# Kernel tuning notes

Hardware: AMD Instinct MI355X
Metric: run time of the kernel (lower is better)

The kernel has to match this reference:

```python
import jax, jax.numpy as jnp
import numpy as np

TEMPERATURE = 0.07  # init kwarg 'temperature'


def setup_inputs() -> dict:
    key = jax.random.key(0)
    k1, k2, k3 = jax.random.split(key, 3)
    N, E = 8192, 128
    return {
        "audio_embeds": jax.random.normal(k1, (N, E), dtype=jnp.float32),
        "text_embeds": jax.random.normal(k2, (N, E), dtype=jnp.float32),
        "fids": jax.random.randint(k3, (N,), 0, 4096),
    }


def reference(audio_embeds, text_embeds, fids):
    # Per-sample loop in the original is equivalent to a full NxN score matrix
    # with a symmetric fid-equality mask (diagonal always kept):
    #   row i valid set  = {j : fid[j] != fid[i]} U {i}
    # L_it(i) = CE over S[i, valid] with target i  (A_i vs sampled texts)
    # L_ai(i) = CE over S[valid, i] with target i  (sampled audios vs T_i)
    S = jnp.matmul(audio_embeds, text_embeds.T) / TEMPERATURE  # [N, N], S[j, i] = <A_j, T_i>/t
    N = S.shape[0]
    mask = (fids[:, None] != fids[None, :]) | jnp.eye(N, dtype=bool)  # symmetric
    neg = jnp.finfo(S.dtype).min
    Sm = jnp.where(mask, S, neg)
    diag = jnp.diagonal(S)
    L_it = jax.nn.logsumexp(Sm, axis=1) - diag  # row-wise CE at diagonal target
    L_ai = jax.nn.logsumexp(Sm, axis=0) - diag  # column-wise CE at diagonal target
    return jnp.mean(L_ai + L_it)
```

## Files before the change

kernel.cpp:

```cpp
#include <hip/hip_runtime.h>
#include <hip/hip_bf16.h>
#include <math.h>

#define NN 8192
#define EE 128

static constexpr float INV_T = 1.0f / 0.07f;
static constexpr float LOG2E = 1.4426950408889634f;
static constexpr float LN2   = 0.6931471805599453f;
static constexpr float SENT  = -3.0e38f;

typedef __attribute__((ext_vector_type(8))) short fragAB;
typedef __attribute__((ext_vector_type(4))) float f32x4;
typedef const __attribute__((address_space(1))) void gvoid;
typedef __attribute__((address_space(3))) void lvoid;

__device__ inline float fexp2(float x) { float r; asm("v_exp_f32 %0, %1" : "=v"(r) : "v"(x)); return r; }
__device__ inline float flog2(float x) { float r; asm("v_log_f32 %0, %1" : "=v"(r) : "v"(x)); return r; }

template<int CTRL>
__device__ inline float dpp_f(float x) {
  return __builtin_bit_cast(float,
      __builtin_amdgcn_update_dpp(0, __builtin_bit_cast(int, x), CTRL, 0xf, 0xf, true));
}
__device__ inline float red16_max(float x) {
  x = fmaxf(x, dpp_f<0xB1>(x));
  x = fmaxf(x, dpp_f<0x4E>(x));
  x = fmaxf(x, dpp_f<0x141>(x));
  x = fmaxf(x, dpp_f<0x140>(x));
  return x;
}
__device__ inline float red16_add(float x) {
  x += dpp_f<0xB1>(x); x += dpp_f<0x4E>(x); x += dpp_f<0x141>(x); x += dpp_f<0x140>(x);
  return x;
}

__device__ inline ushort f32_to_bf16_bits(float x) {
  union { float f; unsigned u; } c; c.f = x;
  unsigned u = c.u;
  u += 0x7fffu + ((u >> 16) & 1u);
  return (ushort)(u >> 16);
}

__global__ void lsl_cvt_kernel(const float* __restrict__ A, const float* __restrict__ T,
                               ushort* __restrict__ Ab, ushort* __restrict__ Tb,
                               float* __restrict__ diag) {
  const int t = blockIdx.x * 256 + threadIdx.x;
  const int i = t * 4;
  float4 a = *reinterpret_cast<const float4*>(A + i);
  float4 tt = *reinterpret_cast<const float4*>(T + i);
  ushort4 oa, ot;
  const float SC = INV_T * LOG2E;
  oa.x = f32_to_bf16_bits(a.x * SC); oa.y = f32_to_bf16_bits(a.y * SC);
  oa.z = f32_to_bf16_bits(a.z * SC); oa.w = f32_to_bf16_bits(a.w * SC);
  ot.x = f32_to_bf16_bits(tt.x); ot.y = f32_to_bf16_bits(tt.y);
  ot.z = f32_to_bf16_bits(tt.z); ot.w = f32_to_bf16_bits(tt.w);
  *reinterpret_cast<ushort4*>(Ab + i) = oa;
  *reinterpret_cast<ushort4*>(Tb + i) = ot;

  float pd = a.x * tt.x + a.y * tt.y + a.z * tt.z + a.w * tt.w;
  pd += __shfl_xor(pd, 1); pd += __shfl_xor(pd, 2); pd += __shfl_xor(pd, 4);
  pd += __shfl_xor(pd, 8); pd += __shfl_xor(pd, 16);
  if ((threadIdx.x & 31) == 0) diag[i >> 7] = pd * (INV_T * LOG2E);
}

#define MMAC(av, bv)                                                              \
  _Pragma("unroll") for (int fm = 0; fm < 4; ++fm)                                \
    _Pragma("unroll") for (int fn = 0; fn < 4; ++fn)                              \
      acc[fm][fn] = __builtin_amdgcn_mfma_f32_16x16x32_bf16(av[fm], bv[fn], acc[fm][fn], 0, 0, 0);

__global__ __launch_bounds__(256) void
lsl_tile_kernel(const ushort* __restrict__ Ab, const ushort* __restrict__ Tb,
                const int* __restrict__ fids,
                float2* __restrict__ rowp, float2* __restrict__ colp) {
  __shared__ ushort As[128 * 128];
  __shared__ ushort Bs[128 * 128];

  const int bid = blockIdx.x;
  const int swz = (bid & 7) * 512 + (bid >> 3);
  const int tm = swz >> 6, tn = swz & 63;
  const int tid = threadIdx.x;
  const int lane = tid & 63;
  const int wid  = tid >> 6;
  const int wm = wid >> 1, wn = wid & 1;
  const int rbase = tm * 128 + wm * 64;
  const int cbase = tn * 128 + wn * 64;
  const int lr = lane & 15, lg = lane >> 4;

  {
    const int trow = tid >> 4;
    const int scol = ((tid & 15) ^ trow) * 8;
    const ushort* gA = Ab + (size_t)(tm * 128 + trow) * EE + scol;
    const ushort* gB = Tb + (size_t)(tn * 128 + trow) * EE + scol;
#pragma unroll
    for (int i = 0; i < 8; ++i)
      __builtin_amdgcn_global_load_lds((gvoid*)(gA + (size_t)i * 16 * EE),
          (lvoid*)((char*)As + i * 4096 + wid * 1024), 16, 0, 0);
#pragma unroll
    for (int i = 0; i < 8; ++i)
      __builtin_amdgcn_global_load_lds((gvoid*)(gB + (size_t)i * 16 * EE),
          (lvoid*)((char*)Bs + i * 4096 + wid * 1024), 16, 0, 0);
  }
  __syncthreads();

  f32x4 acc[4][4] = {};
#pragma unroll
  for (int ks = 0; ks < 4; ++ks) {
    fragAB av[4], bv[4];
#pragma unroll
    for (int f = 0; f < 4; ++f) {
      av[f] = *reinterpret_cast<const fragAB*>(
          &As[(wm * 64 + f * 16 + lr) * 128 + (((ks * 4 + lg) ^ lr) * 8)]);
      bv[f] = *reinterpret_cast<const fragAB*>(
          &Bs[(wn * 64 + f * 16 + lr) * 128 + (((ks * 4 + lg) ^ lr) * 8)]);
    }
    MMAC(av, bv)
  }

  int fr[4][4], fc[4];
#pragma unroll
  for (int fm = 0; fm < 4; ++fm) {
    int4 v4 = *reinterpret_cast<const int4*>(fids + rbase + fm * 16 + lg * 4);
    fr[fm][0] = v4.x; fr[fm][1] = v4.y; fr[fm][2] = v4.z; fr[fm][3] = v4.w;
  }
#pragma unroll
  for (int fn = 0; fn < 4; ++fn) fc[fn] = fids[cbase + fn * 16 + lr];

  float e[4][4][4];
  const bool diagtile = (rbase == cbase);
#pragma unroll
  for (int fm = 0; fm < 4; ++fm)
#pragma unroll
    for (int fn = 0; fn < 4; ++fn)
#pragma unroll
      for (int r = 0; r < 4; ++r) {
        float v = acc[fm][fn][r];
        bool keep = (fr[fm][r] != fc[fn]) || (diagtile && fm == fn && lr == lg * 4 + r);
        e[fm][fn][r] = keep ? v : SENT;
      }

  float rm[4][4];
#pragma unroll
  for (int fm = 0; fm < 4; ++fm)
#pragma unroll
    for (int r = 0; r < 4; ++r)
      rm[fm][r] = fmaxf(fmaxf(e[fm][0][r], e[fm][1][r]),
                        fmaxf(e[fm][2][r], e[fm][3][r]));
#pragma unroll
  for (int fm = 0; fm < 4; ++fm)
#pragma unroll
    for (int r = 0; r < 4; ++r)
      rm[fm][r] = red16_max(rm[fm][r]);

  float rs[4][4];
#pragma unroll
  for (int fm = 0; fm < 4; ++fm)
#pragma unroll
    for (int r = 0; r < 4; ++r)
      rs[fm][r] = (fexp2(e[fm][0][r] - rm[fm][r]) + fexp2(e[fm][1][r] - rm[fm][r]))
                + (fexp2(e[fm][2][r] - rm[fm][r]) + fexp2(e[fm][3][r] - rm[fm][r]));
#pragma unroll
  for (int fm = 0; fm < 4; ++fm)
#pragma unroll
    for (int r = 0; r < 4; ++r)
      rs[fm][r] = red16_add(rs[fm][r]);

  const int rblk = tn * 2 + wn;
  if (lr == 0) {
#pragma unroll
    for (int fm = 0; fm < 4; ++fm)
#pragma unroll
      for (int r = 0; r < 4; ++r)
        rowp[(size_t)rblk * NN + (rbase + fm * 16 + lg * 4 + r)] = make_float2(rm[fm][r], rs[fm][r]);
  }

  float cm[4];
#pragma unroll
  for (int fn = 0; fn < 4; ++fn) {
    float m0 = fmaxf(fmaxf(e[0][fn][0], e[0][fn][1]), fmaxf(e[0][fn][2], e[0][fn][3]));
    float m1 = fmaxf(fmaxf(e[1][fn][0], e[1][fn][1]), fmaxf(e[1][fn][2], e[1][fn][3]));
    float m2 = fmaxf(fmaxf(e[2][fn][0], e[2][fn][1]), fmaxf(e[2][fn][2], e[2][fn][3]));
    float m3 = fmaxf(fmaxf(e[3][fn][0], e[3][fn][1]), fmaxf(e[3][fn][2], e[3][fn][3]));
    cm[fn] = fmaxf(fmaxf(m0, m1), fmaxf(m2, m3));
  }
  {
    float t0 = __shfl_xor(cm[0], 16), t1 = __shfl_xor(cm[1], 16),
          t2 = __shfl_xor(cm[2], 16), t3 = __shfl_xor(cm[3], 16);
    cm[0] = fmaxf(cm[0], t0); cm[1] = fmaxf(cm[1], t1);
    cm[2] = fmaxf(cm[2], t2); cm[3] = fmaxf(cm[3], t3);
    t0 = __shfl_xor(cm[0], 32); t1 = __shfl_xor(cm[1], 32);
    t2 = __shfl_xor(cm[2], 32); t3 = __shfl_xor(cm[3], 32);
    cm[0] = fmaxf(cm[0], t0); cm[1] = fmaxf(cm[1], t1);
    cm[2] = fmaxf(cm[2], t2); cm[3] = fmaxf(cm[3], t3);
  }
  float cs[4];
#pragma unroll
  for (int fn = 0; fn < 4; ++fn) {
    float s0 = (fexp2(e[0][fn][0] - cm[fn]) + fexp2(e[0][fn][1] - cm[fn]))
             + (fexp2(e[0][fn][2] - cm[fn]) + fexp2(e[0][fn][3] - cm[fn]));
    float s1 = (fexp2(e[1][fn][0] - cm[fn]) + fexp2(e[1][fn][1] - cm[fn]))
             + (fexp2(e[1][fn][2] - cm[fn]) + fexp2(e[1][fn][3] - cm[fn]));
    float s2 = (fexp2(e[2][fn][0] - cm[fn]) + fexp2(e[2][fn][1] - cm[fn]))
             + (fexp2(e[2][fn][2] - cm[fn]) + fexp2(e[2][fn][3] - cm[fn]));
    float s3 = (fexp2(e[3][fn][0] - cm[fn]) + fexp2(e[3][fn][1] - cm[fn]))
             + (fexp2(e[3][fn][2] - cm[fn]) + fexp2(e[3][fn][3] - cm[fn]));
    cs[fn] = (s0 + s1) + (s2 + s3);
  }
  {
    float t0 = __shfl_xor(cs[0], 16), t1 = __shfl_xor(cs[1], 16),
          t2 = __shfl_xor(cs[2], 16), t3 = __shfl_xor(cs[3], 16);
    cs[0] += t0; cs[1] += t1; cs[2] += t2; cs[3] += t3;
    t0 = __shfl_xor(cs[0], 32); t1 = __shfl_xor(cs[1], 32);
    t2 = __shfl_xor(cs[2], 32); t3 = __shfl_xor(cs[3], 32);
    cs[0] += t0; cs[1] += t1; cs[2] += t2; cs[3] += t3;
  }

  const int cblk = tm * 2 + wm;
  if (lg == 0) {
#pragma unroll
    for (int fn = 0; fn < 4; ++fn)
      colp[(size_t)cblk * NN + (cbase + fn * 16 + lr)] = make_float2(cm[fn], cs[fn]);
  }
}

__global__ __launch_bounds__(256) void
lsl_merge_kernel(const float2* __restrict__ rowp, const float2* __restrict__ colp,
                 const float* __restrict__ diag, float* __restrict__ bsum) {
  __shared__ float2 sl[128 * 33];
  __shared__ float2 red[32][8];
  const int tid = threadIdx.x;
  const int ibase = blockIdx.x * 32;
  const int s = tid & 31, p = tid >> 5;

  float lse0 = 0.f, lse1 = 0.f;
#pragma unroll
  for (int pass = 0; pass < 2; ++pass) {
    const float2* __restrict__ src = pass ? colp : rowp;
#pragma unroll
    for (int k = 0; k < 16; ++k) {
      int L = tid + k * 256;
      int b = L >> 5, di = L & 31;
      sl[b * 33 + di] = src[(size_t)b * NN + ibase + di];
    }
    __syncthreads();
    float m = SENT;
#pragma unroll
    for (int k = 0; k < 16; ++k) m = fmaxf(m, sl[(p * 16 + k) * 33 + s].x);
    float sum = 0.f;
#pragma unroll
    for (int k = 0; k < 16; ++k) {
      float2 v = sl[(p * 16 + k) * 33 + s];
      sum += v.y * fexp2(v.x - m);
    }
    red[s][p] = make_float2(m, sum);
    __syncthreads();
    if (p == 0) {
      float M = SENT;
#pragma unroll
      for (int k = 0; k < 8; ++k) M = fmaxf(M, red[s][k].x);
      float S = 0.f;
#pragma unroll
      for (int k = 0; k < 8; ++k) S += red[s][k].y * fexp2(red[s][k].x - M);
      if (pass == 0) lse0 = M + flog2(S); else lse1 = M + flog2(S);
    }
    __syncthreads();
  }

  if (tid < 32) {
    float loss = lse0 + lse1 - 2.f * diag[ibase + tid];
#pragma unroll
    for (int d = 1; d < 32; d <<= 1) loss += __shfl_xor(loss, d);
    if (tid == 0) bsum[blockIdx.x] = loss;
  }
}

__global__ __launch_bounds__(256) void
lsl_final_kernel(const float* __restrict__ bsum, float* __restrict__ out) {
  float v = bsum[threadIdx.x];
#pragma unroll
  for (int d = 1; d < 64; d <<= 1) v += __shfl_xor(v, d);
  __shared__ float l4[4];
  if ((threadIdx.x & 63) == 0) l4[threadIdx.x >> 6] = v;
  __syncthreads();
  if (threadIdx.x == 0) out[0] = (l4[0] + l4[1] + l4[2] + l4[3]) * (LN2 / (float)NN);
}

extern "C" void kernel_launch(void* const* d_in, const int* in_sizes, int n_in,
                              void* d_out, int out_size, void* d_ws, size_t ws_size,
                              hipStream_t stream) {
  const float* A = (const float*)d_in[0];
  const float* T = (const float*)d_in[1];
  const int* fids = (const int*)d_in[2];
  float* out = (float*)d_out;
  char* ws = (char*)d_ws;

  size_t off = 0;
  ushort* Ab  = (ushort*)(ws + off); off += (size_t)NN * EE * 2;
  ushort* Tb  = (ushort*)(ws + off); off += (size_t)NN * EE * 2;
  float* diag = (float*)(ws + off);  off += (size_t)NN * 4;
  float2* rowp = (float2*)(ws + off); off += (size_t)NN * 128 * 8;
  float2* colp = (float2*)(ws + off); off += (size_t)NN * 128 * 8;
  float* bsum = (float*)(ws + off);  off += 1024;

  hipLaunchKernelGGL(lsl_cvt_kernel, dim3(NN * EE / 4 / 256), dim3(256), 0, stream, A, T, Ab, Tb, diag);
  hipLaunchKernelGGL(lsl_tile_kernel, dim3(4096), dim3(256), 0, stream, Ab, Tb, fids, rowp, colp);
  hipLaunchKernelGGL(lsl_merge_kernel, dim3(NN / 32), dim3(256), 0, stream, rowp, colp, diag, bsum);
  hipLaunchKernelGGL(lsl_final_kernel, dim3(1), dim3(256), 0, stream, bsum, out);
}
```

Measured before the change: 62.36 us.

## Split 128x128 tile across 8 waves with LDS merge of column partials

Raises the tile kernel from 4 to 8 waves per block. Each wave now computes a 32x64 sub-tile instead of 64x64, which halves the accumulator and exp work per wave and the registers it needs. Column partial max/sum pairs from the two waves sharing a column block are combined through a small shared-memory buffer with an extra barrier, so the colp layout stays the same. The aim is more latency hiding and occupancy. The cost is more B-fragment LDS reads per output and an extra sync.

Result: slower. 63.65 us (+2.1%).

```diff
diff --git a/kernel.cpp b/kernel.cpp
--- a/kernel.cpp
+++ b/kernel.cpp
@@ -64,17 +64,13 @@
   if ((threadIdx.x & 31) == 0) diag[i >> 7] = pd * (INV_T * LOG2E);
 }
 
-#define MMAC(av, bv)                                                              \
-  _Pragma("unroll") for (int fm = 0; fm < 4; ++fm)                                \
-    _Pragma("unroll") for (int fn = 0; fn < 4; ++fn)                              \
-      acc[fm][fn] = __builtin_amdgcn_mfma_f32_16x16x32_bf16(av[fm], bv[fn], acc[fm][fn], 0, 0, 0);
-
-__global__ __launch_bounds__(256) void
+__global__ __launch_bounds__(512, 4) void
 lsl_tile_kernel(const ushort* __restrict__ Ab, const ushort* __restrict__ Tb,
                 const int* __restrict__ fids,
                 float2* __restrict__ rowp, float2* __restrict__ colp) {
   __shared__ ushort As[128 * 128];
   __shared__ ushort Bs[128 * 128];
+  __shared__ float2 cscr[4 * 64];
 
   const int bid = blockIdx.x;
   const int swz = (bid & 7) * 512 + (bid >> 3);
@@ -82,85 +78,92 @@
   const int tid = threadIdx.x;
   const int lane = tid & 63;
   const int wid  = tid >> 6;
-  const int wm = wid >> 1, wn = wid & 1;
-  const int rbase = tm * 128 + wm * 64;
+  const int wm = wid >> 1;
+  const int wn = wid & 1;
+  const int rbase = tm * 128 + wm * 32;
   const int cbase = tn * 128 + wn * 64;
   const int lr = lane & 15, lg = lane >> 4;
 
   {
     const int trow = tid >> 4;
-    const int scol = ((tid & 15) ^ trow) * 8;
+    const int scol = ((tid & 15) ^ (trow & 15)) * 8;
     const ushort* gA = Ab + (size_t)(tm * 128 + trow) * EE + scol;
     const ushort* gB = Tb + (size_t)(tn * 128 + trow) * EE + scol;
 #pragma unroll
-    for (int i = 0; i < 8; ++i)
-      __builtin_amdgcn_global_load_lds((gvoid*)(gA + (size_t)i * 16 * EE),
-          (lvoid*)((char*)As + i * 4096 + wid * 1024), 16, 0, 0);
-#pragma unroll
-    for (int i = 0; i < 8; ++i)
-      __builtin_amdgcn_global_load_lds((gvoid*)(gB + (size_t)i * 16 * EE),
-          (lvoid*)((char*)Bs + i * 4096 + wid * 1024), 16, 0, 0);
+    for (int i = 0; i < 4; ++i)
+      __builtin_amdgcn_global_load_lds((gvoid*)(gA + (size_t)i * 32 * EE),
+          (lvoid*)((char*)As + i * 8192 + wid * 1024), 16, 0, 0);
+#pragma unroll
+    for (int i = 0; i < 4; ++i)
+      __builtin_amdgcn_global_load_lds((gvoid*)(gB + (size_t)i * 32 * EE),
+          (lvoid*)((char*)Bs + i * 8192 + wid * 1024), 16, 0, 0);
   }
   __syncthreads();
 
-  f32x4 acc[4][4] = {};
+  f32x4 acc[2][4] = {};
 #pragma unroll
   for (int ks = 0; ks < 4; ++ks) {
-    fragAB av[4], bv[4];
-#pragma unroll
-    for (int f = 0; f < 4; ++f) {
+    fragAB av[2], bv[4];
+#pragma unroll
+    for (int f = 0; f < 2; ++f)
       av[f] = *reinterpret_cast<const fragAB*>(
-          &As[(wm * 64 + f * 16 + lr) * 128 + (((ks * 4 + lg) ^ lr) * 8)]);
+          &As[(wm * 32 + f * 16 + lr) * 128 + (((ks * 4 + lg) ^ lr) * 8)]);
+#pragma unroll
+    for (int f = 0; f < 4; ++f)
       bv[f] = *reinterpret_cast<const fragAB*>(
           &Bs[(wn * 64 + f * 16 + lr) * 128 + (((ks * 4 + lg) ^ lr) * 8)]);
-    }
-    MMAC(av, bv)
-  }
-
-  int fr[4][4], fc[4];
-#pragma unroll
-  for (int fm = 0; fm < 4; ++fm) {
+#pragma unroll
+    for (int fm = 0; fm < 2; ++fm)
+#pragma unroll
+      for (int fn = 0; fn < 4; ++fn)
+        acc[fm][fn] = __builtin_amdgcn_mfma_f32_16x16x32_bf16(av[fm], bv[fn], acc[fm][fn], 0, 0, 0);
+  }
+
+  int fr[2][4], fc[4];
+#pragma unroll
+  for (int fm = 0; fm < 2; ++fm) {
     int4 v4 = *reinterpret_cast<const int4*>(fids + rbase + fm * 16 + lg * 4);
     fr[fm][0] = v4.x; fr[fm][1] = v4.y; fr[fm][2] = v4.z; fr[fm][3] = v4.w;
   }
 #pragma unroll
   for (int fn = 0; fn < 4; ++fn) fc[fn] = fids[cbase + fn * 16 + lr];
 
-  float e[4][4][4];
-  const bool diagtile = (rbase == cbase);
-#pragma unroll
-  for (int fm = 0; fm < 4; ++fm)
+  float e[2][4][4];
+  const bool dt = (tm == tn) && ((wm >> 1) == wn);
+  const int dfb = (wm & 1) * 2;
+#pragma unroll
+  for (int fm = 0; fm < 2; ++fm)
 #pragma unroll
     for (int fn = 0; fn < 4; ++fn)
 #pragma unroll
       for (int r = 0; r < 4; ++r) {
         float v = acc[fm][fn][r];
-        bool keep = (fr[fm][r] != fc[fn]) || (diagtile && fm == fn && lr == lg * 4 + r);
+        bool keep = (fr[fm][r] != fc[fn]) || (dt && fn == dfb + fm && lr == lg * 4 + r);
         e[fm][fn][r] = keep ? v : SENT;
       }
 
-  float rm[4][4];
-#pragma unroll
-  for (int fm = 0; fm < 4; ++fm)
+  float rm[2][4];
+#pragma unroll
+  for (int fm = 0; fm < 2; ++fm)
 #pragma unroll
     for (int r = 0; r < 4; ++r)
       rm[fm][r] = fmaxf(fmaxf(e[fm][0][r], e[fm][1][r]),
                         fmaxf(e[fm][2][r], e[fm][3][r]));
 #pragma unroll
-  for (int fm = 0; fm < 4; ++fm)
+  for (int fm = 0; fm < 2; ++fm)
 #pragma unroll
     for (int r = 0; r < 4; ++r)
       rm[fm][r] = red16_max(rm[fm][r]);
 
-  float rs[4][4];
-#pragma unroll
-  for (int fm = 0; fm < 4; ++fm)
+  float rs[2][4];
+#pragma unroll
+  for (int fm = 0; fm < 2; ++fm)
 #pragma unroll
     for (int r = 0; r < 4; ++r)
       rs[fm][r] = (fexp2(e[fm][0][r] - rm[fm][r]) + fexp2(e[fm][1][r] - rm[fm][r]))
                 + (fexp2(e[fm][2][r] - rm[fm][r]) + fexp2(e[fm][3][r] - rm[fm][r]));
 #pragma unroll
-  for (int fm = 0; fm < 4; ++fm)
+  for (int fm = 0; fm < 2; ++fm)
 #pragma unroll
     for (int r = 0; r < 4; ++r)
       rs[fm][r] = red16_add(rs[fm][r]);
@@ -168,7 +171,7 @@
   const int rblk = tn * 2 + wn;
   if (lr == 0) {
 #pragma unroll
-    for (int fm = 0; fm < 4; ++fm)
+    for (int fm = 0; fm < 2; ++fm)
 #pragma unroll
       for (int r = 0; r < 4; ++r)
         rowp[(size_t)rblk * NN + (rbase + fm * 16 + lg * 4 + r)] = make_float2(rm[fm][r], rs[fm][r]);
@@ -179,9 +182,7 @@
   for (int fn = 0; fn < 4; ++fn) {
     float m0 = fmaxf(fmaxf(e[0][fn][0], e[0][fn][1]), fmaxf(e[0][fn][2], e[0][fn][3]));
     float m1 = fmaxf(fmaxf(e[1][fn][0], e[1][fn][1]), fmaxf(e[1][fn][2], e[1][fn][3]));
-    float m2 = fmaxf(fmaxf(e[2][fn][0], e[2][fn][1]), fmaxf(e[2][fn][2], e[2][fn][3]));
-    float m3 = fmaxf(fmaxf(e[3][fn][0], e[3][fn][1]), fmaxf(e[3][fn][2], e[3][fn][3]));
-    cm[fn] = fmaxf(fmaxf(m0, m1), fmaxf(m2, m3));
+    cm[fn] = fmaxf(m0, m1);
   }
   {
     float t0 = __shfl_xor(cm[0], 16), t1 = __shfl_xor(cm[1], 16),
@@ -200,11 +201,7 @@
              + (fexp2(e[0][fn][2] - cm[fn]) + fexp2(e[0][fn][3] - cm[fn]));
     float s1 = (fexp2(e[1][fn][0] - cm[fn]) + fexp2(e[1][fn][1] - cm[fn]))
              + (fexp2(e[1][fn][2] - cm[fn]) + fexp2(e[1][fn][3] - cm[fn]));
-    float s2 = (fexp2(e[2][fn][0] - cm[fn]) + fexp2(e[2][fn][1] - cm[fn]))
-             + (fexp2(e[2][fn][2] - cm[fn]) + fexp2(e[2][fn][3] - cm[fn]));
-    float s3 = (fexp2(e[3][fn][0] - cm[fn]) + fexp2(e[3][fn][1] - cm[fn]))
-             + (fexp2(e[3][fn][2] - cm[fn]) + fexp2(e[3][fn][3] - cm[fn]));
-    cs[fn] = (s0 + s1) + (s2 + s3);
+    cs[fn] = s0 + s1;
   }
   {
     float t0 = __shfl_xor(cs[0], 16), t1 = __shfl_xor(cs[1], 16),
@@ -215,11 +212,22 @@
     cs[0] += t0; cs[1] += t1; cs[2] += t2; cs[3] += t3;
   }
 
-  const int cblk = tm * 2 + wm;
-  if (lg == 0) {
+  const int pi = (wm >> 1) * 2 + wn;
+  if ((wm & 1) == 1 && lg == 0) {
 #pragma unroll
     for (int fn = 0; fn < 4; ++fn)
-      colp[(size_t)cblk * NN + (cbase + fn * 16 + lr)] = make_float2(cm[fn], cs[fn]);
+      cscr[pi * 64 + fn * 16 + lr] = make_float2(cm[fn], cs[fn]);
+  }
+  __syncthreads();
+  if ((wm & 1) == 0 && lg == 0) {
+    const int cblk = tm * 2 + (wm >> 1);
+#pragma unroll
+    for (int fn = 0; fn < 4; ++fn) {
+      float2 o = cscr[pi * 64 + fn * 16 + lr];
+      float M = fmaxf(cm[fn], o.x);
+      float S = cs[fn] * fexp2(cm[fn] - M) + o.y * fexp2(o.x - M);
+      colp[(size_t)cblk * NN + (cbase + fn * 16 + lr)] = make_float2(M, S);
+    }
   }
 }
 
@@ -303,7 +311,7 @@
   float* bsum = (float*)(ws + off);  off += 1024;
 
   hipLaunchKernelGGL(lsl_cvt_kernel, dim3(NN * EE / 4 / 256), dim3(256), 0, stream, A, T, Ab, Tb, diag);
-  hipLaunchKernelGGL(lsl_tile_kernel, dim3(4096), dim3(256), 0, stream, Ab, Tb, fids, rowp, colp);
+  hipLaunchKernelGGL(lsl_tile_kernel, dim3(4096), dim3(512), 0, stream, Ab, Tb, fids, rowp, colp);
   hipLaunchKernelGGL(lsl_merge_kernel, dim3(NN / 32), dim3(256), 0, stream, rowp, colp, diag, bsum);
   hipLaunchKernelGGL(lsl_final_kernel, dim3(1), dim3(256), 0, stream, bsum, out);
 }
```
